# Kernel tuning notes

Measured on AMD Instinct MI355X. Metric: run time of the kernel, lower is better.

## Reference

```python
import jax, jax.numpy as jnp
import numpy as np

N, E = 3000, 96000
IN_C, HID, OUT_C = 512, 256, 64
K1, K2, K3 = 2000, 1000, 500  # ceil(ratio * n) per depth; ratios = [2000/N, 0.5, 0.5]


def gcn_conv(A, x, W, b):
    # GCNConv(improved=True): A_hat = A + 2I, symmetric norm; A[i, j] = weight of edge j -> i
    n = A.shape[0]
    Ah = A + 2.0 * jnp.eye(n, dtype=A.dtype)
    deg = Ah.sum(axis=1)
    dis = jnp.where(deg > 0, jax.lax.rsqrt(deg), 0.0)
    return (dis[:, None] * Ah * dis[None, :]) @ (x @ W) + b


def augment(A):
    # GraphUNet.augment_adj: add self loops, A @ A (spspmm), remove self loops
    n = A.shape[0]
    eye = jnp.eye(n, dtype=A.dtype)
    Ah = A + eye
    return (Ah @ Ah) * (1.0 - eye)


def topk_pool(A, x, w, k):
    # TopKPooling: score = tanh((x @ w) / ||w||); keep top-k nodes, scale feats, take sub-adjacency
    score = jnp.tanh((x @ w) / jnp.linalg.norm(w))
    sv, perm = jax.lax.top_k(score, k)
    return x[perm] * sv[:, None], A[perm][:, perm], perm


def setup_inputs():
    key = jax.random.key(0)
    ks = jax.random.split(key, 16)

    def glorot(k, shape):
        lim = float(np.sqrt(6.0 / (shape[0] + shape[1])))
        return jax.random.uniform(k, shape, jnp.float32, -lim, lim)

    return {
        "x": jax.random.normal(ks[0], (N, IN_C), jnp.float32),
        "edge_index": jax.random.randint(ks[1], (2, E), 0, N, jnp.int32),
        "W0": glorot(ks[2], (IN_C, HID)), "b0": jnp.zeros((HID,), jnp.float32),
        "W1": glorot(ks[3], (HID, HID)), "b1": jnp.zeros((HID,), jnp.float32),
        "W2": glorot(ks[4], (HID, HID)), "b2": jnp.zeros((HID,), jnp.float32),
        "W3": glorot(ks[5], (HID, HID)), "b3": jnp.zeros((HID,), jnp.float32),
        "p1": jax.random.normal(ks[6], (HID,), jnp.float32),
        "p2": jax.random.normal(ks[7], (HID,), jnp.float32),
        "p3": jax.random.normal(ks[8], (HID,), jnp.float32),
        "U0": glorot(ks[9], (HID, HID)), "c0": jnp.zeros((HID,), jnp.float32),
        "U1": glorot(ks[10], (HID, HID)), "c1": jnp.zeros((HID,), jnp.float32),
        "U2": glorot(ks[11], (HID, OUT_C)), "c2": jnp.zeros((OUT_C,), jnp.float32),
    }


def reference(x, edge_index, W0, b0, W1, b1, W2, b2, W3, b3, p1, p2, p3, U0, c0, U1, c1, U2, c2):
    # eval mode: dropout_edge(p=0.2) and F.dropout(p=0.92) are identity
    relu = jax.nn.relu
    src, dst = edge_index[0], edge_index[1]
    A = jnp.zeros((N, N), x.dtype).at[dst, src].add(1.0)  # dense adjacency, coalesces duplicates

    x0 = relu(gcn_conv(A, x, W0, b0))                     # down conv 0 on original graph
    x1in, A1, perm1 = topk_pool(augment(A), x0, p1, K1)
    x1 = relu(gcn_conv(A1, x1in, W1, b1))
    x2in, A2, perm2 = topk_pool(augment(A1), x1, p2, K2)
    x2 = relu(gcn_conv(A2, x2in, W2, b2))
    x3in, A3, perm3 = topk_pool(augment(A2), x2, p3, K3)
    x3 = relu(gcn_conv(A3, x3in, W3, b3))

    h = x2 + jnp.zeros_like(x2).at[perm3].set(x3)         # unpool + sum residual
    h = relu(gcn_conv(A2, h, U0, c0))
    h = x1 + jnp.zeros_like(x1).at[perm2].set(h)
    h = relu(gcn_conv(A1, h, U1, c1))
    h = x0 + jnp.zeros_like(x0).at[perm1].set(h)
    h = gcn_conv(A, h, U2, c2)                            # final up conv, no activation
    return jax.nn.log_softmax(h, axis=1)
```

## Files before the change

### kernel.cpp

```cpp
#include <hip/hip_runtime.h>
#include <math.h>
#include <stdint.h>

#define N0   3000
#define NE   96000
#define INC  512
#define HIDF 256
#define OUTC 64
#define KP1  2000
#define KP2  1000
#define KP3  500
#define KP1P 2048
#define KP2P 1024
#define KP3P 512

typedef __bf16 bf16x8 __attribute__((ext_vector_type(8)));
typedef float f32x4 __attribute__((ext_vector_type(4)));

#define GLDS16(gp, lp)                                                   \
  __builtin_amdgcn_global_load_lds(                                      \
      (__attribute__((address_space(1))) void*)(gp),                     \
      (__attribute__((address_space(3))) void*)(lp), 16, 0, 0)

static __global__ void count_k(const int* __restrict__ ei, int* __restrict__ cd) {
  int e = blockIdx.x * blockDim.x + threadIdx.x;
  if (e < NE) atomicAdd(&cd[ei[NE + e]], 1);
}

static __global__ __launch_bounds__(1024) void scan_excl_k(const int* __restrict__ cnt,
                                                           int* __restrict__ start, int n,
                                                           float* __restrict__ dis0) {
  __shared__ int s[4096];
  int tid = threadIdx.x;
  for (int i = tid; i < 4096; i += blockDim.x) s[i] = (i < n) ? cnt[i] : 0;
  __syncthreads();
  for (int d = 1; d < 4096; d <<= 1) {
    int v[4]; int r = 0;
    for (int i = tid; i < 4096; i += blockDim.x, ++r) v[r] = (i >= d) ? s[i - d] : 0;
    __syncthreads();
    r = 0;
    for (int i = tid; i < 4096; i += blockDim.x, ++r) s[i] += v[r];
    __syncthreads();
  }
  for (int i = tid; i < n; i += blockDim.x) {
    start[i] = (i == 0) ? 0 : s[i - 1];
    dis0[i] = rsqrtf((float)cnt[i] + 2.0f);
  }
  if (tid == 0) start[n] = s[n - 1];
}

static __global__ void scatter_k(const int* __restrict__ ei, const int* __restrict__ sd,
                                 int* __restrict__ fd, int* __restrict__ bd) {
  int e = blockIdx.x * blockDim.x + threadIdx.x;
  if (e < NE) {
    int d = ei[NE + e];
    bd[sd[d] + atomicAdd(&fd[d], 1)] = ei[e];
  }
}

static __global__ __launch_bounds__(256) void augA_masked_k(
    const int* __restrict__ st, const int* __restrict__ bk,
    const int* __restrict__ perm, const int* __restrict__ pos,
    __bf16* __restrict__ A1bf, float* __restrict__ dis1) {
  __shared__ float row[KP1];
  __shared__ float sh[4];
  int tid = threadIdx.x, lane = tid & 63, wave = tid >> 6;
  int r = blockIdx.x;
  int vi = perm[r];
  for (int c = tid; c < KP1; c += 256) row[c] = 0.f;
  __syncthreads();
  int b = st[vi], e = st[vi + 1];
  for (int t = b + wave; t < e; t += 4) {
    int k = bk[t];
    int jb = st[k], je = st[k + 1];
    for (int u = jb + lane; u < je; u += 64) {
      int p = pos[bk[u]];
      if (p >= 0) atomicAdd(&row[p], 1.0f);
    }
  }
  if (wave == 0)
    for (int t = b + lane; t < e; t += 64) {
      int p = pos[bk[t]];
      if (p >= 0) atomicAdd(&row[p], 2.0f);
    }
  __syncthreads();
  if (tid == 0) row[r] = 0.f;
  __syncthreads();
  float s = 0.f;
  for (int c = tid; c < KP1P; c += 256) {
    float v = (c < KP1) ? row[c] : 0.f;
    A1bf[(size_t)r * KP1P + c] = (__bf16)v;
    s += v;
  }
#pragma unroll
  for (int o = 32; o > 0; o >>= 1) s += __shfl_down(s, o, 64);
  if (lane == 0) sh[wave] = s;
  __syncthreads();
  if (tid == 0) dis1[r] = rsqrtf(sh[0] + sh[1] + sh[2] + sh[3] + 2.0f);
}

static __global__ void spmm_sc_k(const int* __restrict__ start, const int* __restrict__ idx,
                                 const float* __restrict__ xw, const float* __restrict__ dis,
                                 float* __restrict__ out, int F) {
  int row = blockIdx.x;
  int b = start[row], e = start[row + 1];
  int f = threadIdx.x;
  __shared__ int nb[256];
  __shared__ float nd[256];
  float acc = 0.f;
  for (int t0 = b; t0 < e; t0 += blockDim.x) {
    int m = min((int)blockDim.x, e - t0);
    __syncthreads();
    if (f < m) { int s = idx[t0 + f]; nb[f] = s; nd[f] = dis[s]; }
    __syncthreads();
    for (int t = 0; t < m; ++t) acc += xw[(size_t)nb[t] * F + f] * nd[t];
  }
  out[(size_t)row * F + f] = acc;
}

static __global__ void conv_hilo_k(const float* __restrict__ in, int R, int C, int Cp,
                                   __bf16* __restrict__ oh, __bf16* __restrict__ ol) {
  int idx = blockIdx.x * blockDim.x + threadIdx.x;
  if (idx < R * Cp) {
    int r = idx / Cp, c = idx - r * Cp;
    float v = (c < C) ? in[(size_t)r * C + c] : 0.f;
    __bf16 h = (__bf16)v;
    oh[idx] = h;
    if (ol) ol[idx] = (__bf16)(v - (float)h);
  }
}

struct TDesc { const float* in; __bf16* oh; __bf16* ol; int R, C, Rp; };
struct TDescs { TDesc d[7]; };
static __global__ __launch_bounds__(256) void wtconv_k(TDescs ds) {
  TDesc d = ds.d[blockIdx.z];
  int r0 = blockIdx.x * 32, c0 = blockIdx.y * 32;
  if (r0 >= d.Rp || c0 >= d.C) return;
  __shared__ float t[32][33];
  int lr = threadIdx.x >> 5, lc = threadIdx.x & 31;
#pragma unroll
  for (int i = 0; i < 4; ++i) {
    int r = r0 + lr + i * 8, c = c0 + lc;
    t[lr + i * 8][lc] = (r < d.R && c < d.C) ? d.in[(size_t)r * d.C + c] : 0.f;
  }
  __syncthreads();
#pragma unroll
  for (int i = 0; i < 4; ++i) {
    int c = c0 + lr + i * 8, r = r0 + lc;
    if (c < d.C) {
      float v = t[lc][lr + i * 8];
      __bf16 h = (__bf16)v;
      d.oh[(size_t)c * d.Rp + r] = h;
      d.ol[(size_t)c * d.Rp + r] = (__bf16)(v - (float)h);
    }
  }
}

static __global__ __launch_bounds__(256) void btrans_k(const __bf16* __restrict__ ih,
                                                       const __bf16* __restrict__ il,
                                                       __bf16* __restrict__ oh, __bf16* __restrict__ ol,
                                                       int Rin, int Ls, int Cout, int Lo) {
  __shared__ __bf16 th[32][40], tl[32][40];
  int r0 = blockIdx.x * 32, c0 = blockIdx.y * 32;
  int lr = threadIdx.x >> 5, lc = threadIdx.x & 31;
#pragma unroll
  for (int i = 0; i < 4; ++i) {
    int r = r0 + lr + i * 8, c = c0 + lc;
    bool ok = (r < Rin);
    th[lr + i * 8][lc] = ok ? ih[(size_t)r * Ls + c] : (__bf16)0.f;
    if (il) tl[lr + i * 8][lc] = ok ? il[(size_t)r * Ls + c] : (__bf16)0.f;
  }
  __syncthreads();
#pragma unroll
  for (int i = 0; i < 4; ++i) {
    int c = c0 + lr + i * 8, r = r0 + lc;
    if (c < Cout) {
      oh[(size_t)c * Lo + r] = th[lc][lr + i * 8];
      if (ol) ol[(size_t)c * Lo + r] = tl[lc][lr + i * 8];
    }
  }
}

static __global__ __launch_bounds__(256) void redtconv_k(const float* __restrict__ Cp, int ks, int mn,
                                                         int R, int C, int Rp,
                                                         __bf16* __restrict__ oh, __bf16* __restrict__ ol,
                                                         const float* __restrict__ disv,
                                                         float* __restrict__ xw_out) {
  __shared__ float t[32][33];
  int r0 = blockIdx.x * 32, c0 = blockIdx.y * 32;
  int lr = threadIdx.x >> 5, lc = threadIdx.x & 31;
#pragma unroll
  for (int i = 0; i < 4; ++i) {
    int r = r0 + lr + i * 8, c = c0 + lc;
    float v = 0.f;
    if (r < R && c < C) {
      size_t idx = (size_t)r * C + c;
      for (int z = 0; z < ks; ++z) v += Cp[(size_t)z * mn + idx];
      if (xw_out) xw_out[idx] = v;
    }
    t[lr + i * 8][lc] = v;
  }
  __syncthreads();
#pragma unroll
  for (int i = 0; i < 4; ++i) {
    int c = c0 + lr + i * 8, r = r0 + lc;
    if (c < C) {
      float v = t[lc][lr + i * 8];
      if (r < R) v *= disv[r];
      __bf16 h = (__bf16)v;
      oh[(size_t)c * Rp + r] = h;
      ol[(size_t)c * Rp + r] = (__bf16)(v - (float)h);
    }
  }
}

static __global__ void ghilo_k(const float* __restrict__ src, const int* __restrict__ perm,
                               const float* __restrict__ sv, __bf16* __restrict__ oh,
                               __bf16* __restrict__ ol, int k) {
  int idx = blockIdx.x * blockDim.x + threadIdx.x;
  if (idx < k * HIDF) {
    int r = idx >> 8;
    float v = src[(size_t)perm[r] * HIDF + (idx & 255)] * sv[r];
    __bf16 h = (__bf16)v;
    oh[idx] = h;
    ol[idx] = (__bf16)(v - (float)h);
  }
}

template <int BM, int BN>
static __global__ __launch_bounds__(256) void mgemm_k(
    const __bf16* __restrict__ A0, const __bf16* __restrict__ A1g, const __bf16* __restrict__ A2g,
    const __bf16* __restrict__ B0, const __bf16* __restrict__ B1g, const __bf16* __restrict__ B2g,
    const int* __restrict__ pA, const int* __restrict__ pB,
    int nseg, float* __restrict__ Cp, int M, int N, int Kp, int kchunk) {
  constexpr int FM = BM / 32, FN = BN / 32;
  __shared__ __bf16 As[2][BM * 64];
  __shared__ __bf16 Bs[2][BN * 64];
  int tid = threadIdx.x;
  int lane = tid & 63, wave = tid >> 6;
  int wx = wave & 1, wy = wave >> 1;
  int l15 = lane & 15, l4 = lane >> 4;
  int brow = blockIdx.y * BM, bcol = blockIdx.x * BN;
  int wrow = wy * (BM / 2), wcol = wx * (BN / 2);
  int srow = lane >> 3, slot = lane & 7;
  int k_beg = blockIdx.z * kchunk;
  int ksteps = kchunk >> 6;
  int nsteps = nseg * ksteps;
  const __bf16* segA[3] = {A0, A1g, A2g};
  const __bf16* segB[3] = {B0, B1g, B2g};

  int rowA[BM / 32], rowB[BN / 32];
#pragma unroll
  for (int i = 0; i < BM / 32; ++i) {
    int rl = (i * 4 + wave) * 8 + srow;
    int gr = brow + rl;
    if (gr >= M) gr = M - 1;
    rowA[i] = pA ? pA[gr] : gr;
  }
#pragma unroll
  for (int i = 0; i < BN / 32; ++i) {
    int rl = (i * 4 + wave) * 8 + srow;
    int gc = bcol + rl;
    if (gc >= N) gc = N - 1;
    rowB[i] = pB ? pB[gc] : gc;
  }

  auto stage = [&](int buf, int t) {
    int seg = t / ksteps;
    int k0 = k_beg + ((t - seg * ksteps) << 6);
    const __bf16* Ag = segA[seg];
    const __bf16* Bg = segB[seg];
#pragma unroll
    for (int i = 0; i < BM / 32; ++i) {
      int rl = (i * 4 + wave) * 8 + srow;
      int col = k0 + ((slot ^ (rl & 7)) << 3);
      GLDS16(Ag + (size_t)rowA[i] * Kp + col, &As[buf][(i * 4 + wave) * 8 * 64]);
    }
#pragma unroll
    for (int i = 0; i < BN / 32; ++i) {
      int rl = (i * 4 + wave) * 8 + srow;
      int col = k0 + ((slot ^ (rl & 7)) << 3);
      GLDS16(Bg + (size_t)rowB[i] * Kp + col, &Bs[buf][(i * 4 + wave) * 8 * 64]);
    }
  };

  f32x4 acc[FM][FN] = {};
  stage(0, 0);
  __syncthreads();
  int cur = 0;
  for (int t = 0; t < nsteps; ++t) {
    if (t + 1 < nsteps) stage(cur ^ 1, t + 1);
#pragma unroll
    for (int sub = 0; sub < 2; ++sub) {
      bf16x8 af[FM], bfv[FN];
#pragma unroll
      for (int i = 0; i < FM; ++i) {
        int r = wrow + i * 16 + l15;
        af[i] = *(const bf16x8*)(&As[cur][r * 64 + (((sub * 4 + l4) ^ (r & 7)) << 3)]);
      }
#pragma unroll
      for (int j = 0; j < FN; ++j) {
        int r = wcol + j * 16 + l15;
        bfv[j] = *(const bf16x8*)(&Bs[cur][r * 64 + (((sub * 4 + l4) ^ (r & 7)) << 3)]);
      }
#pragma unroll
      for (int i = 0; i < FM; ++i)
#pragma unroll
        for (int j = 0; j < FN; ++j)
          acc[i][j] = __builtin_amdgcn_mfma_f32_16x16x32_bf16(af[i], bfv[j], acc[i][j], 0, 0, 0);
    }
    __syncthreads();
    cur ^= 1;
  }
  size_t zoff = (size_t)blockIdx.z * M * N;
#pragma unroll
  for (int i = 0; i < FM; ++i)
#pragma unroll
    for (int j = 0; j < FN; ++j) {
      int col = bcol + wcol + j * 16 + l15;
      if (col < N) {
#pragma unroll
        for (int q = 0; q < 4; ++q) {
          int row = brow + wrow + i * 16 + l4 * 4 + q;
          if (row < M) Cp[zoff + (size_t)row * N + col] = acc[i][j][q];
        }
      }
    }
}

static __global__ __launch_bounds__(256) void epi_score_k(
    const float* __restrict__ zp, int ks, int mn, const float* __restrict__ xw,
    const float* __restrict__ disv, const float* __restrict__ bias,
    const float* __restrict__ p, float* __restrict__ outx, float* __restrict__ sc) {
  int r = blockIdx.x, tid = threadIdx.x;
  size_t idx = (size_t)r * HIDF + tid;
  float zv = 0.f;
  for (int z = 0; z < ks; ++z) zv += zp[(size_t)z * mn + idx];
  float di = disv[r];
  float v = di * zv + 2.0f * di * di * xw[idx] + bias[tid];
  v = fmaxf(v, 0.0f);
  outx[idx] = v;
  float wv = p[tid];
  float s = v * wv, q = wv * wv;
  __shared__ float sh[4], sh2[4];
  int lane = tid & 63, wid = tid >> 6;
#pragma unroll
  for (int o = 32; o > 0; o >>= 1) { s += __shfl_down(s, o, 64); q += __shfl_down(q, o, 64); }
  if (lane == 0) { sh[wid] = s; sh2[wid] = q; }
  __syncthreads();
  if (tid == 0)
    sc[r] = tanhf((sh[0] + sh[1] + sh[2] + sh[3]) / sqrtf(sh2[0] + sh2[1] + sh2[2] + sh2[3]));
}

static __global__ void unpool_epi_k(const float* __restrict__ base, const float* __restrict__ zp,
                                    int ks, int mn, const float* __restrict__ xwp,
                                    const float* __restrict__ disv, const float* __restrict__ bias,
                                    const int* __restrict__ pos, __bf16* __restrict__ oh,
                                    __bf16* __restrict__ ol, int n) {
  int idx = blockIdx.x * blockDim.x + threadIdx.x;
  if (idx < n * HIDF) {
    int i = idx >> 8, j = idx & 255;
    int p = pos[i];
    float v = base[idx];
    if (p >= 0) {
      size_t pidx = (size_t)p * HIDF + j;
      float zv = 0.f;
      for (int z = 0; z < ks; ++z) zv += zp[(size_t)z * mn + pidx];
      float di = disv[p];
      float u = di * zv + 2.0f * di * di * xwp[pidx] + bias[j];
      v += fmaxf(u, 0.0f);
    }
    __bf16 h = (__bf16)v;
    oh[idx] = h;
    ol[idx] = (__bf16)(v - (float)h);
  }
}

static __global__ __launch_bounds__(256) void aug_epi_k(
    const float* __restrict__ Cp, int ks, int mn, int n, int dstL,
    const __bf16* __restrict__ srcH, const __bf16* __restrict__ srcL, int srcLen,
    const int* __restrict__ permv, __bf16* __restrict__ bh, __bf16* __restrict__ bl,
    float* __restrict__ dis) {
  __shared__ int pm[1000];
  __shared__ float srow[2048];
  __shared__ float sh[4];
  int r = blockIdx.x;
  int tid = threadIdx.x, lane = tid & 63, wave = tid >> 6;
  int vi = permv[r];
  for (int c = tid; c < n; c += 256) pm[c] = permv[c];
  for (int k = tid; k < srcLen; k += 256) {
    float v = (float)srcH[(size_t)vi * srcLen + k];
    if (srcL) v += (float)srcL[(size_t)vi * srcLen + k];
    srow[k] = v;
  }
  __syncthreads();
  float ssum = 0.f;
  for (int c = tid; c < dstL; c += 256) {
    float v = 0.f;
    if (c < n && c != r) {
      for (int z = 0; z < ks; ++z) v += Cp[(size_t)z * mn + (size_t)r * n + c];
      v += 2.0f * srow[pm[c]];
    }
    __bf16 h = (__bf16)v;
    bh[(size_t)r * dstL + c] = h;
    bl[(size_t)r * dstL + c] = (__bf16)(v - (float)h);
    ssum += v;
  }
#pragma unroll
  for (int o = 32; o > 0; o >>= 1) ssum += __shfl_down(ssum, o, 64);
  if (lane == 0) sh[wave] = ssum;
  __syncthreads();
  if (tid == 0) dis[r] = rsqrtf(sh[0] + sh[1] + sh[2] + sh[3] + 2.0f);
}

static __global__ __launch_bounds__(256) void topk_rank_k(const float* __restrict__ sc, int n, int k,
                                                          int* __restrict__ perm, float* __restrict__ sv,
                                                          int* __restrict__ pos) {
  __shared__ float s[N0 + 8];
  int tid = threadIdx.x, lane = tid & 63, wave = tid >> 6;
  for (int i = tid; i < n; i += 256) s[i] = sc[i];
  __syncthreads();
  int i = blockIdx.x * 4 + wave;
  if (i < n) {
    float si = s[i];
    int rank = 0;
    for (int j = lane; j < n; j += 64) {
      float sj = s[j];
      rank += (sj > si) || (sj == si && j < i);
    }
#pragma unroll
    for (int o = 32; o > 0; o >>= 1) rank += __shfl_down(rank, o, 64);
    if (lane == 0) {
      pos[i] = (rank < k) ? rank : -1;
      if (rank < k) { perm[rank] = i; sv[rank] = si; }
    }
  }
}

static __global__ void epilsm_k(const float* __restrict__ zb, const float* __restrict__ xw,
                                const float* __restrict__ dis, const float* __restrict__ b,
                                float* __restrict__ out) {
  int r = blockIdx.x, j = threadIdx.x;
  float di = dis[r];
  float v = di * zb[r * OUTC + j] + 2.0f * di * di * xw[r * OUTC + j] + b[j];
  float m = v;
#pragma unroll
  for (int o = 32; o > 0; o >>= 1) m = fmaxf(m, __shfl_xor(m, o, 64));
  float e = expf(v - m), s = e;
#pragma unroll
  for (int o = 32; o > 0; o >>= 1) s += __shfl_xor(s, o, 64);
  out[r * OUTC + j] = v - m - logf(s);
}

extern "C" void kernel_launch(void* const* d_in, const int* in_sizes, int n_in,
                              void* d_out, int out_size, void* d_ws, size_t ws_size,
                              hipStream_t stream) {
  const float* x  = (const float*)d_in[0];
  const int* ei   = (const int*)d_in[1];
  const float* W0 = (const float*)d_in[2];
  const float* b0 = (const float*)d_in[3];
  const float* W1 = (const float*)d_in[4];
  const float* b1 = (const float*)d_in[5];
  const float* W2 = (const float*)d_in[6];
  const float* b2 = (const float*)d_in[7];
  const float* W3 = (const float*)d_in[8];
  const float* b3 = (const float*)d_in[9];
  const float* p1 = (const float*)d_in[10];
  const float* p2 = (const float*)d_in[11];
  const float* p3 = (const float*)d_in[12];
  const float* U0 = (const float*)d_in[13];
  const float* c0 = (const float*)d_in[14];
  const float* U1 = (const float*)d_in[15];
  const float* c1 = (const float*)d_in[16];
  const float* U2 = (const float*)d_in[17];
  const float* c2 = (const float*)d_in[18];
  (void)in_sizes; (void)n_in; (void)out_size; (void)ws_size;

  char* basep = (char*)d_ws;
  size_t off = 0;
  auto alloc = [&](size_t bytes) {
    void* p = basep + off;
    off += (bytes + 255) & ~(size_t)255;
    return p;
  };

  float* xw  = (float*)alloc((size_t)N0 * HIDF * 4);
  float* zb  = (float*)alloc((size_t)N0 * HIDF * 4);
  float* x0  = (float*)alloc((size_t)N0 * HIDF * 4);
  float* x1  = (float*)alloc((size_t)KP1 * HIDF * 4);
  float* x2  = (float*)alloc((size_t)KP2 * HIDF * 4);
  float* Cpart = (float*)alloc((size_t)20 * 1024 * 1024);
  __bf16* bfAh = (__bf16*)alloc((size_t)N0 * INC * 2);
  __bf16* bfAl = (__bf16*)alloc((size_t)N0 * INC * 2);
  __bf16* bfBh = (__bf16*)alloc((size_t)HIDF * KP1P * 2);
  __bf16* bfBl = (__bf16*)alloc((size_t)HIDF * KP1P * 2);
  __bf16* A1bf  = (__bf16*)alloc((size_t)KP1 * KP1P * 2);
  __bf16* A1tbf = (__bf16*)alloc((size_t)KP1 * KP1P * 2);
  __bf16* A2bh  = (__bf16*)alloc((size_t)KP2 * KP2P * 2);
  __bf16* A2bl  = (__bf16*)alloc((size_t)KP2 * KP2P * 2);
  __bf16* A2tbh = (__bf16*)alloc((size_t)KP2 * KP2P * 2);
  __bf16* A2tbl = (__bf16*)alloc((size_t)KP2 * KP2P * 2);
  __bf16* A3bh  = (__bf16*)alloc((size_t)KP3 * KP3P * 2);
  __bf16* A3bl  = (__bf16*)alloc((size_t)KP3 * KP3P * 2);
  __bf16* w0h = (__bf16*)alloc((size_t)HIDF * 512 * 2);
  __bf16* w0l = (__bf16*)alloc((size_t)HIDF * 512 * 2);
  __bf16* w1h = (__bf16*)alloc((size_t)HIDF * 256 * 2);
  __bf16* w1l = (__bf16*)alloc((size_t)HIDF * 256 * 2);
  __bf16* w2h = (__bf16*)alloc((size_t)HIDF * 256 * 2);
  __bf16* w2l = (__bf16*)alloc((size_t)HIDF * 256 * 2);
  __bf16* w3h = (__bf16*)alloc((size_t)HIDF * 256 * 2);
  __bf16* w3l = (__bf16*)alloc((size_t)HIDF * 256 * 2);
  __bf16* u0h = (__bf16*)alloc((size_t)HIDF * 256 * 2);
  __bf16* u0l = (__bf16*)alloc((size_t)HIDF * 256 * 2);
  __bf16* u1h = (__bf16*)alloc((size_t)HIDF * 256 * 2);
  __bf16* u1l = (__bf16*)alloc((size_t)HIDF * 256 * 2);
  __bf16* u2h = (__bf16*)alloc((size_t)OUTC * 256 * 2);
  __bf16* u2l = (__bf16*)alloc((size_t)OUTC * 256 * 2);
  float* sc   = (float*)alloc(N0 * 4);
  float* sv   = (float*)alloc(KP1 * 4);
  int* perm1  = (int*)alloc(KP1 * 4);
  int* perm2  = (int*)alloc(KP2 * 4);
  int* perm3  = (int*)alloc(KP3 * 4);
  int* pos1   = (int*)alloc(N0 * 4);
  int* pos2   = (int*)alloc(KP1 * 4);
  int* pos3   = (int*)alloc(KP2 * 4);
  float* dis0 = (float*)alloc(N0 * 4);
  float* dis1 = (float*)alloc(KP1 * 4);
  float* dis2 = (float*)alloc(KP2 * 4);
  float* dis3 = (float*)alloc(KP3 * 4);
  int* cf     = (int*)alloc((size_t)2 * 3072 * 4);
  int* cnt_d  = cf;
  int* fl_d   = cf + 3072;
  int* st_d   = (int*)alloc((N0 + 4) * 4);
  int* bk_d   = (int*)alloc(NE * 4);

  auto mg = [&](int bm, int bn, const __bf16* a0, const __bf16* a1, const __bf16* a2,
                const __bf16* bb0, const __bf16* bb1, const __bf16* bb2,
                const int* pA, const int* pB, int nseg, float* Cdst,
                int M, int N, int Kp, int ks, int kchunk) {
    dim3 g((N + bn - 1) / bn, (M + bm - 1) / bm, ks);
    if (bm == 128 && bn == 128)
      mgemm_k<128, 128><<<g, 256, 0, stream>>>(a0, a1, a2, bb0, bb1, bb2, pA, pB, nseg, Cdst, M, N, Kp, kchunk);
    else if (bm == 128)
      mgemm_k<128, 64><<<g, 256, 0, stream>>>(a0, a1, a2, bb0, bb1, bb2, pA, pB, nseg, Cdst, M, N, Kp, kchunk);
    else
      mgemm_k<64, 64><<<g, 256, 0, stream>>>(a0, a1, a2, bb0, bb1, bb2, pA, pB, nseg, Cdst, M, N, Kp, kchunk);
  };

  auto wgemm = [&](const __bf16* wh, const __bf16* wl, int fin, int fout, int n) {
    int Kp = (fin + 63) & ~63;
    mg(64, 64, bfAh, bfAh, bfAl, wh, wl, wh, nullptr, nullptr, 3, xw, n, fout, Kp, 1, Kp);
  };

  auto propg = [&](const __bf16* Abh, const __bf16* Abl, int asegs, int n, int Kp, int bm,
                   int ks, int kchunk, const float* disv) {
    dim3 tg(Kp / 32, HIDF / 32);
    redtconv_k<<<tg, 256, 0, stream>>>(xw, 1, 0, n, HIDF, Kp, bfBh, bfBl, disv, nullptr);
    if (asegs == 1) mg(bm, 64, Abh, Abh, nullptr, bfBh, bfBl, nullptr, nullptr, nullptr, 2, Cpart, n, HIDF, Kp, ks, kchunk);
    else            mg(bm, 64, Abh, Abh, Abl, bfBh, bfBl, bfBh, nullptr, nullptr, 3, Cpart, n, HIDF, Kp, ks, kchunk);
  };

  hipMemsetAsync(cf, 0, (size_t)2 * 3072 * 4, stream);
  count_k<<<(NE + 255) / 256, 256, 0, stream>>>(ei, cnt_d);
  {
    TDescs ds;
    ds.d[0] = {W0, w0h, w0l, INC, HIDF, 512};
    ds.d[1] = {W1, w1h, w1l, HIDF, HIDF, 256};
    ds.d[2] = {W2, w2h, w2l, HIDF, HIDF, 256};
    ds.d[3] = {W3, w3h, w3l, HIDF, HIDF, 256};
    ds.d[4] = {U0, u0h, u0l, HIDF, HIDF, 256};
    ds.d[5] = {U1, u1h, u1l, HIDF, HIDF, 256};
    ds.d[6] = {U2, u2h, u2l, HIDF, OUTC, 256};
    wtconv_k<<<dim3(16, 8, 7), 256, 0, stream>>>(ds);
  }
  scan_excl_k<<<1, 1024, 0, stream>>>(cnt_d, st_d, N0, dis0);
  scatter_k<<<(NE + 255) / 256, 256, 0, stream>>>(ei, st_d, fl_d, bk_d);

  conv_hilo_k<<<((size_t)N0 * INC + 255) / 256, 256, 0, stream>>>(x, N0, INC, INC, bfAh, bfAl);
  wgemm(w0h, w0l, INC, HIDF, N0);
  spmm_sc_k<<<N0, HIDF, 0, stream>>>(st_d, bk_d, xw, dis0, zb, HIDF);
  epi_score_k<<<N0, 256, 0, stream>>>(zb, 1, 0, xw, dis0, b0, p1, x0, sc);
  topk_rank_k<<<(N0 + 3) / 4, 256, 0, stream>>>(sc, N0, KP1, perm1, sv, pos1);

  augA_masked_k<<<KP1, 256, 0, stream>>>(st_d, bk_d, perm1, pos1, A1bf, dis1);

  ghilo_k<<<((size_t)KP1 * HIDF + 255) / 256, 256, 0, stream>>>(x0, perm1, sv, bfAh, bfAl, KP1);
  wgemm(w1h, w1l, HIDF, HIDF, KP1);
  propg(A1bf, nullptr, 1, KP1, KP1P, 128, 4, 512, dis1);
  epi_score_k<<<KP1, 256, 0, stream>>>(Cpart, 4, KP1 * HIDF, xw, dis1, b1, p2, x1, sc);
  topk_rank_k<<<(KP1 + 3) / 4, 256, 0, stream>>>(sc, KP1, KP2, perm2, sv, pos2);

  btrans_k<<<dim3(KP1P / 32, (KP1 + 31) / 32), 256, 0, stream>>>(A1bf, nullptr, A1tbf, nullptr,
                                                                 KP1, KP1P, KP1, KP1P);
  mg(128, 128, A1bf, nullptr, nullptr, A1tbf, nullptr, nullptr, perm2, perm2,
     1, Cpart, KP2, KP2, KP1P, 2, 1024);
  aug_epi_k<<<KP2, 256, 0, stream>>>(Cpart, 2, KP2 * KP2, KP2, KP2P, A1bf, nullptr, KP1P, perm2,
                                     A2bh, A2bl, dis2);

  ghilo_k<<<((size_t)KP2 * HIDF + 255) / 256, 256, 0, stream>>>(x1, perm2, sv, bfAh, bfAl, KP2);
  wgemm(w2h, w2l, HIDF, HIDF, KP2);
  propg(A2bh, A2bl, 2, KP2, KP2P, 128, 4, 256, dis2);
  epi_score_k<<<KP2, 256, 0, stream>>>(Cpart, 4, KP2 * HIDF, xw, dis2, b2, p3, x2, sc);
  topk_rank_k<<<(KP2 + 3) / 4, 256, 0, stream>>>(sc, KP2, KP3, perm3, sv, pos3);

  btrans_k<<<dim3(KP2P / 32, (KP2 + 31) / 32), 256, 0, stream>>>(A2bh, A2bl, A2tbh, A2tbl,
                                                                 KP2, KP2P, KP2, KP2P);
  mg(64, 64, A2bh, A2bh, A2bl, A2tbh, A2tbl, A2tbh, perm3, perm3, 3, Cpart, KP3, KP3, KP2P, 2, 512);
  aug_epi_k<<<KP3, 256, 0, stream>>>(Cpart, 2, KP3 * KP3, KP3, KP3P, A2bh, A2bl, KP2P, perm3,
                                     A3bh, A3bl, dis3);

  ghilo_k<<<((size_t)KP3 * HIDF + 255) / 256, 256, 0, stream>>>(x2, perm3, sv, bfAh, bfAl, KP3);
  wgemm(w3h, w3l, HIDF, HIDF, KP3);
  propg(A3bh, A3bl, 2, KP3, KP3P, 64, 4, 128, dis3);
  unpool_epi_k<<<(KP2 * HIDF + 255) / 256, 256, 0, stream>>>(x2, Cpart, 4, KP3 * HIDF, xw, dis3, b3,
                                                             pos3, bfAh, bfAl, KP2);

  wgemm(u0h, u0l, HIDF, HIDF, KP2);
  propg(A2bh, A2bl, 2, KP2, KP2P, 128, 4, 256, dis2);
  unpool_epi_k<<<(KP1 * HIDF + 255) / 256, 256, 0, stream>>>(x1, Cpart, 4, KP2 * HIDF, xw, dis2, c0,
                                                             pos2, bfAh, bfAl, KP1);

  wgemm(u1h, u1l, HIDF, HIDF, KP1);
  propg(A1bf, nullptr, 1, KP1, KP1P, 128, 4, 512, dis1);
  unpool_epi_k<<<(N0 * HIDF + 255) / 256, 256, 0, stream>>>(x0, Cpart, 4, KP1 * HIDF, xw, dis1, c1,
                                                            pos1, bfAh, bfAl, N0);

  wgemm(u2h, u2l, HIDF, OUTC, N0);
  spmm_sc_k<<<N0, OUTC, 0, stream>>>(st_d, bk_d, xw, dis0, zb, OUTC);
  epilsm_k<<<N0, OUTC, 0, stream>>>(zb, xw, dis0, c2, (float*)d_out);
}
```

Baseline: 459.1 us.

## Fold self-loop term into adjacency diagonal and retune split-K GEMM tiling

The 2I self-loop contribution is now stored on the adjacency diagonal (and as an initial accumulator term in the sparse SpMM) instead of being added separately in every epilogue. This removes the extra xw reads from the epilogue kernels and the xw copy in the transpose kernel. The propagation and augmentation GEMMs also switch to a new 64x128 or 128x128 tile shape with more split-K chunks, so the partial-sum reductions read more partials. The diagonal value of 2 is now routed through bf16 hi/lo storage and the GEMM, which changes rounding slightly.

New measurement: 439.6 us. 4.2% less time.

```diff
diff --git a/kernel.cpp b/kernel.cpp
--- a/kernel.cpp
+++ b/kernel.cpp
@@ -84,7 +84,7 @@
       if (p >= 0) atomicAdd(&row[p], 2.0f);
     }
   __syncthreads();
-  if (tid == 0) row[r] = 0.f;
+  if (tid == 0) row[r] = 2.0f;
   __syncthreads();
   float s = 0.f;
   for (int c = tid; c < KP1P; c += 256) {
@@ -96,7 +96,7 @@
   for (int o = 32; o > 0; o >>= 1) s += __shfl_down(s, o, 64);
   if (lane == 0) sh[wave] = s;
   __syncthreads();
-  if (tid == 0) dis1[r] = rsqrtf(sh[0] + sh[1] + sh[2] + sh[3] + 2.0f);
+  if (tid == 0) dis1[r] = rsqrtf(sh[0] + sh[1] + sh[2] + sh[3]);
 }
 
 static __global__ void spmm_sc_k(const int* __restrict__ start, const int* __restrict__ idx,
@@ -107,7 +107,7 @@
   int f = threadIdx.x;
   __shared__ int nb[256];
   __shared__ float nd[256];
-  float acc = 0.f;
+  float acc = 2.0f * dis[row] * xw[(size_t)row * F + f];
   for (int t0 = b; t0 < e; t0 += blockDim.x) {
     int m = min((int)blockDim.x, e - t0);
     __syncthreads();
@@ -184,8 +184,7 @@
 static __global__ __launch_bounds__(256) void redtconv_k(const float* __restrict__ Cp, int ks, int mn,
                                                          int R, int C, int Rp,
                                                          __bf16* __restrict__ oh, __bf16* __restrict__ ol,
-                                                         const float* __restrict__ disv,
-                                                         float* __restrict__ xw_out) {
+                                                         const float* __restrict__ disv) {
   __shared__ float t[32][33];
   int r0 = blockIdx.x * 32, c0 = blockIdx.y * 32;
   int lr = threadIdx.x >> 5, lc = threadIdx.x & 31;
@@ -196,7 +195,6 @@
     if (r < R && c < C) {
       size_t idx = (size_t)r * C + c;
       for (int z = 0; z < ks; ++z) v += Cp[(size_t)z * mn + idx];
-      if (xw_out) xw_out[idx] = v;
     }
     t[lr + i * 8][lc] = v;
   }
@@ -329,16 +327,14 @@
 }
 
 static __global__ __launch_bounds__(256) void epi_score_k(
-    const float* __restrict__ zp, int ks, int mn, const float* __restrict__ xw,
+    const float* __restrict__ zp, int ks, int mn,
     const float* __restrict__ disv, const float* __restrict__ bias,
     const float* __restrict__ p, float* __restrict__ outx, float* __restrict__ sc) {
   int r = blockIdx.x, tid = threadIdx.x;
   size_t idx = (size_t)r * HIDF + tid;
   float zv = 0.f;
   for (int z = 0; z < ks; ++z) zv += zp[(size_t)z * mn + idx];
-  float di = disv[r];
-  float v = di * zv + 2.0f * di * di * xw[idx] + bias[tid];
-  v = fmaxf(v, 0.0f);
+  float v = fmaxf(disv[r] * zv + bias[tid], 0.0f);
   outx[idx] = v;
   float wv = p[tid];
   float s = v * wv, q = wv * wv;
@@ -353,7 +349,7 @@
 }
 
 static __global__ void unpool_epi_k(const float* __restrict__ base, const float* __restrict__ zp,
-                                    int ks, int mn, const float* __restrict__ xwp,
+                                    int ks, int mn,
                                     const float* __restrict__ disv, const float* __restrict__ bias,
                                     const int* __restrict__ pos, __bf16* __restrict__ oh,
                                     __bf16* __restrict__ ol, int n) {
@@ -366,9 +362,7 @@
       size_t pidx = (size_t)p * HIDF + j;
       float zv = 0.f;
       for (int z = 0; z < ks; ++z) zv += zp[(size_t)z * mn + pidx];
-      float di = disv[p];
-      float u = di * zv + 2.0f * di * di * xwp[pidx] + bias[j];
-      v += fmaxf(u, 0.0f);
+      v += fmaxf(disv[p] * zv + bias[j], 0.0f);
     }
     __bf16 h = (__bf16)v;
     oh[idx] = h;
@@ -397,9 +391,13 @@
   float ssum = 0.f;
   for (int c = tid; c < dstL; c += 256) {
     float v = 0.f;
-    if (c < n && c != r) {
-      for (int z = 0; z < ks; ++z) v += Cp[(size_t)z * mn + (size_t)r * n + c];
-      v += 2.0f * srow[pm[c]];
+    if (c < n) {
+      if (c == r) {
+        v = 2.0f;
+      } else {
+        for (int z = 0; z < ks; ++z) v += Cp[(size_t)z * mn + (size_t)r * n + c];
+        v -= 2.0f * srow[pm[c]];
+      }
     }
     __bf16 h = (__bf16)v;
     bh[(size_t)r * dstL + c] = h;
@@ -410,7 +408,7 @@
   for (int o = 32; o > 0; o >>= 1) ssum += __shfl_down(ssum, o, 64);
   if (lane == 0) sh[wave] = ssum;
   __syncthreads();
-  if (tid == 0) dis[r] = rsqrtf(sh[0] + sh[1] + sh[2] + sh[3] + 2.0f);
+  if (tid == 0) dis[r] = rsqrtf(sh[0] + sh[1] + sh[2] + sh[3]);
 }
 
 static __global__ __launch_bounds__(256) void topk_rank_k(const float* __restrict__ sc, int n, int k,
@@ -437,12 +435,10 @@
   }
 }
 
-static __global__ void epilsm_k(const float* __restrict__ zb, const float* __restrict__ xw,
-                                const float* __restrict__ dis, const float* __restrict__ b,
-                                float* __restrict__ out) {
+static __global__ void epilsm_k(const float* __restrict__ zb, const float* __restrict__ dis,
+                                const float* __restrict__ b, float* __restrict__ out) {
   int r = blockIdx.x, j = threadIdx.x;
-  float di = dis[r];
-  float v = di * zb[r * OUTC + j] + 2.0f * di * di * xw[r * OUTC + j] + b[j];
+  float v = dis[r] * zb[r * OUTC + j] + b[j];
   float m = v;
 #pragma unroll
   for (int o = 32; o > 0; o >>= 1) m = fmaxf(m, __shfl_xor(m, o, 64));
@@ -543,6 +539,8 @@
       mgemm_k<128, 128><<<g, 256, 0, stream>>>(a0, a1, a2, bb0, bb1, bb2, pA, pB, nseg, Cdst, M, N, Kp, kchunk);
     else if (bm == 128)
       mgemm_k<128, 64><<<g, 256, 0, stream>>>(a0, a1, a2, bb0, bb1, bb2, pA, pB, nseg, Cdst, M, N, Kp, kchunk);
+    else if (bn == 128)
+      mgemm_k<64, 128><<<g, 256, 0, stream>>>(a0, a1, a2, bb0, bb1, bb2, pA, pB, nseg, Cdst, M, N, Kp, kchunk);
     else
       mgemm_k<64, 64><<<g, 256, 0, stream>>>(a0, a1, a2, bb0, bb1, bb2, pA, pB, nseg, Cdst, M, N, Kp, kchunk);
   };
@@ -552,12 +550,12 @@
     mg(64, 64, bfAh, bfAh, bfAl, wh, wl, wh, nullptr, nullptr, 3, xw, n, fout, Kp, 1, Kp);
   };
 
-  auto propg = [&](const __bf16* Abh, const __bf16* Abl, int asegs, int n, int Kp, int bm,
+  auto propg = [&](const __bf16* Abh, const __bf16* Abl, int asegs, int n, int Kp, int bm, int bn,
                    int ks, int kchunk, const float* disv) {
     dim3 tg(Kp / 32, HIDF / 32);
-    redtconv_k<<<tg, 256, 0, stream>>>(xw, 1, 0, n, HIDF, Kp, bfBh, bfBl, disv, nullptr);
-    if (asegs == 1) mg(bm, 64, Abh, Abh, nullptr, bfBh, bfBl, nullptr, nullptr, nullptr, 2, Cpart, n, HIDF, Kp, ks, kchunk);
-    else            mg(bm, 64, Abh, Abh, Abl, bfBh, bfBl, bfBh, nullptr, nullptr, 3, Cpart, n, HIDF, Kp, ks, kchunk);
+    redtconv_k<<<tg, 256, 0, stream>>>(xw, 1, 0, n, HIDF, Kp, bfBh, bfBl, disv);
+    if (asegs == 1) mg(bm, bn, Abh, Abh, nullptr, bfBh, bfBl, nullptr, nullptr, nullptr, 2, Cpart, n, HIDF, Kp, ks, kchunk);
+    else            mg(bm, bn, Abh, Abh, Abl, bfBh, bfBl, bfBh, nullptr, nullptr, 3, Cpart, n, HIDF, Kp, ks, kchunk);
   };
 
   hipMemsetAsync(cf, 0, (size_t)2 * 3072 * 4, stream);
@@ -579,53 +577,53 @@
   conv_hilo_k<<<((size_t)N0 * INC + 255) / 256, 256, 0, stream>>>(x, N0, INC, INC, bfAh, bfAl);
   wgemm(w0h, w0l, INC, HIDF, N0);
   spmm_sc_k<<<N0, HIDF, 0, stream>>>(st_d, bk_d, xw, dis0, zb, HIDF);
-  epi_score_k<<<N0, 256, 0, stream>>>(zb, 1, 0, xw, dis0, b0, p1, x0, sc);
+  epi_score_k<<<N0, 256, 0, stream>>>(zb, 1, 0, dis0, b0, p1, x0, sc);
   topk_rank_k<<<(N0 + 3) / 4, 256, 0, stream>>>(sc, N0, KP1, perm1, sv, pos1);
 
   augA_masked_k<<<KP1, 256, 0, stream>>>(st_d, bk_d, perm1, pos1, A1bf, dis1);
 
   ghilo_k<<<((size_t)KP1 * HIDF + 255) / 256, 256, 0, stream>>>(x0, perm1, sv, bfAh, bfAl, KP1);
   wgemm(w1h, w1l, HIDF, HIDF, KP1);
-  propg(A1bf, nullptr, 1, KP1, KP1P, 128, 4, 512, dis1);
-  epi_score_k<<<KP1, 256, 0, stream>>>(Cpart, 4, KP1 * HIDF, xw, dis1, b1, p2, x1, sc);
+  propg(A1bf, nullptr, 1, KP1, KP1P, 128, 128, 8, 256, dis1);
+  epi_score_k<<<KP1, 256, 0, stream>>>(Cpart, 8, KP1 * HIDF, dis1, b1, p2, x1, sc);
   topk_rank_k<<<(KP1 + 3) / 4, 256, 0, stream>>>(sc, KP1, KP2, perm2, sv, pos2);
 
   btrans_k<<<dim3(KP1P / 32, (KP1 + 31) / 32), 256, 0, stream>>>(A1bf, nullptr, A1tbf, nullptr,
                                                                  KP1, KP1P, KP1, KP1P);
   mg(128, 128, A1bf, nullptr, nullptr, A1tbf, nullptr, nullptr, perm2, perm2,
-     1, Cpart, KP2, KP2, KP1P, 2, 1024);
-  aug_epi_k<<<KP2, 256, 0, stream>>>(Cpart, 2, KP2 * KP2, KP2, KP2P, A1bf, nullptr, KP1P, perm2,
+     1, Cpart, KP2, KP2, KP1P, 4, 512);
+  aug_epi_k<<<KP2, 256, 0, stream>>>(Cpart, 4, KP2 * KP2, KP2, KP2P, A1bf, nullptr, KP1P, perm2,
                                      A2bh, A2bl, dis2);
 
   ghilo_k<<<((size_t)KP2 * HIDF + 255) / 256, 256, 0, stream>>>(x1, perm2, sv, bfAh, bfAl, KP2);
   wgemm(w2h, w2l, HIDF, HIDF, KP2);
-  propg(A2bh, A2bl, 2, KP2, KP2P, 128, 4, 256, dis2);
-  epi_score_k<<<KP2, 256, 0, stream>>>(Cpart, 4, KP2 * HIDF, xw, dis2, b2, p3, x2, sc);
+  propg(A2bh, A2bl, 2, KP2, KP2P, 64, 128, 8, 128, dis2);
+  epi_score_k<<<KP2, 256, 0, stream>>>(Cpart, 8, KP2 * HIDF, dis2, b2, p3, x2, sc);
   topk_rank_k<<<(KP2 + 3) / 4, 256, 0, stream>>>(sc, KP2, KP3, perm3, sv, pos3);
 
   btrans_k<<<dim3(KP2P / 32, (KP2 + 31) / 32), 256, 0, stream>>>(A2bh, A2bl, A2tbh, A2tbl,
                                                                  KP2, KP2P, KP2, KP2P);
-  mg(64, 64, A2bh, A2bh, A2bl, A2tbh, A2tbl, A2tbh, perm3, perm3, 3, Cpart, KP3, KP3, KP2P, 2, 512);
-  aug_epi_k<<<KP3, 256, 0, stream>>>(Cpart, 2, KP3 * KP3, KP3, KP3P, A2bh, A2bl, KP2P, perm3,
+  mg(64, 64, A2bh, A2bh, A2bl, A2tbh, A2tbl, A2tbh, perm3, perm3, 3, Cpart, KP3, KP3, KP2P, 4, 256);
+  aug_epi_k<<<KP3, 256, 0, stream>>>(Cpart, 4, KP3 * KP3, KP3, KP3P, A2bh, A2bl, KP2P, perm3,
                                      A3bh, A3bl, dis3);
 
   ghilo_k<<<((size_t)KP3 * HIDF + 255) / 256, 256, 0, stream>>>(x2, perm3, sv, bfAh, bfAl, KP3);
   wgemm(w3h, w3l, HIDF, HIDF, KP3);
-  propg(A3bh, A3bl, 2, KP3, KP3P, 64, 4, 128, dis3);
-  unpool_epi_k<<<(KP2 * HIDF + 255) / 256, 256, 0, stream>>>(x2, Cpart, 4, KP3 * HIDF, xw, dis3, b3,
+  propg(A3bh, A3bl, 2, KP3, KP3P, 64, 128, 8, 64, dis3);
+  unpool_epi_k<<<(KP2 * HIDF + 255) / 256, 256, 0, stream>>>(x2, Cpart, 8, KP3 * HIDF, dis3, b3,
                                                              pos3, bfAh, bfAl, KP2);
 
   wgemm(u0h, u0l, HIDF, HIDF, KP2);
-  propg(A2bh, A2bl, 2, KP2, KP2P, 128, 4, 256, dis2);
-  unpool_epi_k<<<(KP1 * HIDF + 255) / 256, 256, 0, stream>>>(x1, Cpart, 4, KP2 * HIDF, xw, dis2, c0,
+  propg(A2bh, A2bl, 2, KP2, KP2P, 64, 128, 8, 128, dis2);
+  unpool_epi_k<<<(KP1 * HIDF + 255) / 256, 256, 0, stream>>>(x1, Cpart, 8, KP2 * HIDF, dis2, c0,
                                                              pos2, bfAh, bfAl, KP1);
 
   wgemm(u1h, u1l, HIDF, HIDF, KP1);
-  propg(A1bf, nullptr, 1, KP1, KP1P, 128, 4, 512, dis1);
-  unpool_epi_k<<<(N0 * HIDF + 255) / 256, 256, 0, stream>>>(x0, Cpart, 4, KP1 * HIDF, xw, dis1, c1,
+  propg(A1bf, nullptr, 1, KP1, KP1P, 128, 128, 8, 256, dis1);
+  unpool_epi_k<<<(N0 * HIDF + 255) / 256, 256, 0, stream>>>(x0, Cpart, 8, KP1 * HIDF, dis1, c1,
                                                             pos1, bfAh, bfAl, N0);
 
   wgemm(u2h, u2l, HIDF, OUTC, N0);
   spmm_sc_k<<<N0, OUTC, 0, stream>>>(st_d, bk_d, xw, dis0, zb, OUTC);
-  epilsm_k<<<N0, OUTC, 0, stream>>>(zb, xw, dis0, c2, (float*)d_out);
-}
+  epilsm_k<<<N0, OUTC, 0, stream>>>(zb, dis0, c2, (float*)d_out);
+}
```
